# Optimization experiments

Measured on AMD Instinct MI355X. Metric: run time of the kernel, lower is better.

Reference implementation:

```python
import jax, jax.numpy as jnp
import numpy as np

B, C, H, W = 16, 512, 32, 32
GROUPS = 8
EPS = 1e-5


def setup_inputs() -> dict:
    key = jax.random.key(0)
    ks = jax.random.split(key, 7)
    s = 1.0 / np.sqrt(C)
    return {
        "x": jax.random.normal(ks[0], (B, C, H, W), dtype=jnp.float32),
        "gamma": jnp.ones((C,), dtype=jnp.float32),
        "beta": jnp.zeros((C,), dtype=jnp.float32),
        "w_qkv": jax.random.normal(ks[1], (3 * C, C), dtype=jnp.float32) * s,
        "b_qkv": jnp.zeros((3 * C,), dtype=jnp.float32),
        "w_proj": jax.random.normal(ks[2], (C, C), dtype=jnp.float32) * s,
        "b_proj": jnp.zeros((C,), dtype=jnp.float32),
    }


def group_norm(x, gamma, beta):
    b, c, h, w = x.shape
    xg = x.reshape(b, GROUPS, c // GROUPS, h, w)
    mean = xg.mean(axis=(2, 3, 4), keepdims=True)
    var = xg.var(axis=(2, 3, 4), keepdims=True)
    xn = ((xg - mean) * jax.lax.rsqrt(var + EPS)).reshape(b, c, h, w)
    return xn * gamma[None, :, None, None] + beta[None, :, None, None]


def reference(x, gamma, beta, w_qkv, b_qkv, w_proj, b_proj):
    b, c, h, w = x.shape
    n = h * w
    hn = group_norm(x, gamma, beta)
    # 1x1 conv == channel matmul: [3C, C] x [B, C, N] -> [B, 3C, N]
    qkv = jnp.einsum('oc,bcn->bon', w_qkv, hn.reshape(b, c, n)) + b_qkv[None, :, None]
    q, k, v = jnp.split(qkv, 3, axis=1)  # each [B, C, N]
    scale = c ** (-0.5)
    # scores [B, N, N]: q^T k
    attn = jax.nn.softmax(jnp.einsum('bcn,bcm->bnm', q, k) * scale, axis=-1)
    out = jnp.einsum('bnm,bcm->bcn', attn, v)  # [B, C, N]
    proj = jnp.einsum('oc,bcn->bon', w_proj, out) + b_proj[None, :, None]
    return x + proj.reshape(b, c, h, w)
```

## Files before the change

kernel.cpp:

```cpp
#include <hip/hip_runtime.h>


#define BATCH 16
#define CCH 512
#define NSP 1024
#define EPSV 1e-5f
#define BK 32
#define HT 4096

typedef short bf16x8 __attribute__((ext_vector_type(8)));
typedef float f32x4 __attribute__((ext_vector_type(4)));

__device__ __forceinline__ unsigned short f2bf(float f) {
    unsigned int u = __float_as_uint(f);
    u += 0x7FFF + ((u >> 16) & 1);
    return (unsigned short)(u >> 16);
}

__device__ __forceinline__ void glds16(const void* g, void* l) {
    __builtin_amdgcn_global_load_lds(
        (const __attribute__((address_space(1))) unsigned int*)g,
        (__attribute__((address_space(3))) unsigned int*)l, 16, 0, 0);
}

#define MEMF asm volatile("" ::: "memory")
#define VMW(n) asm volatile("s_waitcnt vmcnt(" #n ")" ::: "memory")

#define XCD_MAP(GX_LOG2, PER, xv, yv, bv)                 \
    const int lin_ = blockIdx.x;                          \
    const int xcd_ = lin_ & 7;                            \
    int slot_ = lin_ >> 3;                                \
    const int hi_ = (slot_ >= (PER)) ? 1 : 0;             \
    const int bv = xcd_ + 8 * hi_;                        \
    slot_ -= hi_ * (PER);                                 \
    const int xv = slot_ & ((1 << (GX_LOG2)) - 1);        \
    const int yv = slot_ >> (GX_LOG2);

__device__ __forceinline__ void gemm128_loop(
    const unsigned short* __restrict__ Ag, const unsigned short* __restrict__ Bg,
    int astr, int bstr, int ktot, short* Al, short* Bl, f32x4* acc) {
    const int t = threadIdx.x;
    const int w = t >> 6, lane = t & 63;
    const int wr = (w >> 1) * 64, wc = (w & 1) * 64;
    const int fr = lane & 15;
    const int fsw = (((lane >> 4) ^ (fr & 3)) * 8);
    const int r0 = t >> 2;
    const int kc = (((t & 3) ^ (r0 & 3)) * 8);
    const unsigned short* Ap0 = Ag + (size_t)r0 * astr + kc;
    const unsigned short* Ap1 = Ag + (size_t)(r0 + 64) * astr + kc;
    const unsigned short* Bp0 = Bg + (size_t)r0 * bstr + kc;
    const unsigned short* Bp1 = Bg + (size_t)(r0 + 64) * bstr + kc;
    short* Alw = Al + w * 512;
    short* Blw = Bl + w * 512;
    for (int k0 = 0; k0 < ktot; k0 += 64) {
        glds16(Ap0 + k0, Alw);
        glds16(Ap1 + k0, Alw + 2048);
        glds16(Ap0 + k0 + 32, Alw + HT);
        glds16(Ap1 + k0 + 32, Alw + HT + 2048);
        glds16(Bp0 + k0, Blw);
        glds16(Bp1 + k0, Blw + 2048);
        glds16(Bp0 + k0 + 32, Blw + HT);
        glds16(Bp1 + k0 + 32, Blw + HT + 2048);
        __syncthreads();
#pragma unroll
        for (int h = 0; h < 2; h++) {
            const short* Ab = Al + h * HT;
            const short* Bb = Bl + h * HT;
            bf16x8 af[4], bfr[4];
#pragma unroll
            for (int mi = 0; mi < 4; mi++)
                af[mi] = *(const bf16x8*)(Ab + (wr + mi * 16 + fr) * BK + fsw);
#pragma unroll
            for (int ni = 0; ni < 4; ni++)
                bfr[ni] = *(const bf16x8*)(Bb + (wc + ni * 16 + fr) * BK + fsw);
#pragma unroll
            for (int mi = 0; mi < 4; mi++)
#pragma unroll
                for (int ni = 0; ni < 4; ni++)
                    acc[mi * 4 + ni] = __builtin_amdgcn_mfma_f32_16x16x32_bf16(
                        af[mi], bfr[ni], acc[mi * 4 + ni], 0, 0, 0);
        }
        __syncthreads();
    }
}

__device__ __forceinline__ void gemm128_dbuf(
    const unsigned short* __restrict__ Ag, const unsigned short* __restrict__ Bg,
    int astr, int bstr, int ktot, short* L, f32x4* acc) {
    const int t = threadIdx.x;
    const int w = t >> 6, lane = t & 63;
    const int wr = (w >> 1) * 64, wc = (w & 1) * 64;
    const int fr = lane & 15;
    const int fsw = (((lane >> 4) ^ (fr & 3)) * 8);
    const int r0 = t >> 2;
    const int kc = (((t & 3) ^ (r0 & 3)) * 8);
    const unsigned short* Ap0 = Ag + (size_t)r0 * astr + kc;
    const unsigned short* Ap1 = Ag + (size_t)(r0 + 64) * astr + kc;
    const unsigned short* Bp0 = Bg + (size_t)r0 * bstr + kc;
    const unsigned short* Bp1 = Bg + (size_t)(r0 + 64) * bstr + kc;
    short* lw = L + w * 512;

#define STG(bf, kk) do {                                  \
    short* aw_ = lw + (bf) * (4 * HT);                    \
    short* bw_ = aw_ + 2 * HT;                            \
    glds16(Ap0 + (kk), aw_);                              \
    glds16(Ap1 + (kk), aw_ + 2048);                       \
    glds16(Ap0 + (kk) + 32, aw_ + HT);                    \
    glds16(Ap1 + (kk) + 32, aw_ + HT + 2048);             \
    glds16(Bp0 + (kk), bw_);                              \
    glds16(Bp1 + (kk), bw_ + 2048);                       \
    glds16(Bp0 + (kk) + 32, bw_ + HT);                    \
    glds16(Bp1 + (kk) + 32, bw_ + HT + 2048);             \
  } while (0)

#define CMP(bf) do {                                                        \
    _Pragma("unroll")                                                       \
    for (int h = 0; h < 2; h++) {                                           \
        const short* Ab_ = L + (bf) * (4 * HT) + h * HT;                    \
        const short* Bb_ = Ab_ + 2 * HT;                                    \
        bf16x8 af[4], bfr[4];                                               \
        _Pragma("unroll")                                                   \
        for (int mi = 0; mi < 4; mi++)                                      \
            af[mi] = *(const bf16x8*)(Ab_ + (wr + mi * 16 + fr) * BK + fsw);\
        _Pragma("unroll")                                                   \
        for (int ni = 0; ni < 4; ni++)                                      \
            bfr[ni] = *(const bf16x8*)(Bb_ + (wc + ni * 16 + fr) * BK + fsw);\
        _Pragma("unroll")                                                   \
        for (int mi = 0; mi < 4; mi++)                                      \
            _Pragma("unroll")                                               \
            for (int ni = 0; ni < 4; ni++)                                  \
                acc[mi * 4 + ni] = __builtin_amdgcn_mfma_f32_16x16x32_bf16( \
                    af[mi], bfr[ni], acc[mi * 4 + ni], 0, 0, 0);            \
    } } while (0)

    STG(0, 0);
    for (int k0 = 0; k0 < ktot; k0 += 128) {
        STG(1, k0 + 64);
        VMW(8);
        MEMF; __builtin_amdgcn_s_barrier();
        CMP(0);
        MEMF; __builtin_amdgcn_s_barrier();
        const int kb = (k0 + 128 < ktot) ? k0 + 128 : 0;
        STG(0, kb);
        VMW(8);
        MEMF; __builtin_amdgcn_s_barrier();
        CMP(1);
        MEMF; __builtin_amdgcn_s_barrier();
    }
    VMW(0);
#undef STG
#undef CMP
}

#define EPI_SETUP()                                          \
    const int t = threadIdx.x, lane = t & 63, w = t >> 6;    \
    const int wr = (w >> 1) * 64, wc = (w & 1) * 64;         \
    const int fr = lane & 15, rr0 = (lane >> 4) * 4;

#define ACC_INIT(acc)                                        \
    f32x4 acc[16];                                           \
    _Pragma("unroll") for (int i = 0; i < 16; i++)           \
        acc[i] = (f32x4){0.f, 0.f, 0.f, 0.f};

__global__ __launch_bounds__(256) void setup_k(
    const float* __restrict__ x, float* __restrict__ sp,
    const float* __restrict__ wa, unsigned short* __restrict__ oa, int na4,
    const float* __restrict__ wb, unsigned short* __restrict__ ob, int nb4,
    float* __restrict__ Lsum, const float* __restrict__ bqv,
    unsigned short* __restrict__ wv_t, float* __restrict__ puv) {
    const int t = threadIdx.x;
    const int bx = blockIdx.x;
    __shared__ float rs[4], rq[4];
    __shared__ __align__(16) unsigned short Tt[64 * 72];
    if (bx < 512) {
        const int bg = bx >> 2, q = bx & 3;
        const float4* xp = (const float4*)(x + (size_t)bg * 65536 + q * 16384);
        float s = 0.f, qq = 0.f;
#pragma unroll
        for (int i = 0; i < 16; i++) {
            float4 v = xp[t + i * 256];
            s += v.x + v.y + v.z + v.w;
            qq += v.x * v.x + v.y * v.y + v.z * v.z + v.w * v.w;
        }
#pragma unroll
        for (int off = 32; off; off >>= 1) {
            s += __shfl_down(s, off);
            qq += __shfl_down(qq, off);
        }
        const int wave = t >> 6, lane = t & 63;
        if (lane == 0) { rs[wave] = s; rq[wave] = qq; }
        __syncthreads();
        if (t == 0) {
            sp[bx * 2] = rs[0] + rs[1] + rs[2] + rs[3];
            sp[bx * 2 + 1] = rq[0] + rq[1] + rq[2] + rq[3];
        }
    } else if (bx < 1280) {
        int i = (bx - 512) * 256 + t;
        const float* src;
        unsigned short* dst;
        int j;
        if (i < na4) { src = wa; dst = oa; j = i; }
        else { j = i - na4; if (j >= nb4) return; src = wb; dst = ob; }
        float4 v = ((const float4*)src)[j];
        ushort4 o;
        o.x = f2bf(v.x); o.y = f2bf(v.y); o.z = f2bf(v.z); o.w = f2bf(v.w);
        ((ushort4*)dst)[j] = o;
    } else if (bx < 1296) {
        int i = (bx - 1280) * 256 + t;
        ((float4*)Lsum)[i] = (float4){0.f, 0.f, 0.f, 0.f};
    } else if (bx < 1360) {
        const int r = bx - 1296;
        const float* src = wa + (size_t)2 * 512 * 512;
        const int to = (r >> 3) * 64, tc = (r & 7) * 64;
        const int ol = t >> 2, cs = t & 3;
#pragma unroll
        for (int j = 0; j < 4; j++) {
            float4 v = *(const float4*)(src + (size_t)(to + ol) * 512 + tc + cs * 16 + j * 4);
            int c = cs * 16 + j * 4;
            Tt[(c + 0) * 72 + ol] = f2bf(v.x);
            Tt[(c + 1) * 72 + ol] = f2bf(v.y);
            Tt[(c + 2) * 72 + ol] = f2bf(v.z);
            Tt[(c + 3) * 72 + ol] = f2bf(v.w);
        }
        __syncthreads();
        const int cl = t >> 2, os = t & 3;
        unsigned short* d = wv_t + (size_t)(tc + cl) * 512 + to + os * 16;
        const unsigned short* s2 = Tt + cl * 72 + os * 16;
        *(uint4*)d = *(const uint4*)s2;
        *(uint4*)(d + 8) = *(const uint4*)(s2 + 8);
    } else {
        const int o = (bx - 1360) * 256 + t;
        const float* wr_ = wb + (size_t)o * 512;
        const float* bv = bqv + 1024;
        float s = 0.f;
        for (int vv = 0; vv < 512; vv += 4) {
            s += wr_[vv] * bv[vv] + wr_[vv + 1] * bv[vv + 1]
               + wr_[vv + 2] * bv[vv + 2] + wr_[vv + 3] * bv[vv + 3];
        }
        puv[o] = s;
    }
}

__global__ __launch_bounds__(256) void gn_tr_k(
    const float* __restrict__ x, const float* __restrict__ gamma,
    const float* __restrict__ beta, const float* __restrict__ sp,
    unsigned short* __restrict__ hn_t,
    const unsigned short* __restrict__ wp_bf, const unsigned short* __restrict__ wv_t,
    unsigned short* __restrict__ wpv_bf) {
    __shared__ __align__(16) short SM[4 * HT];
    const int lin = blockIdx.x;
    const int t = threadIdx.x;
    if (lin < 16) {
        const int ot = (lin >> 2) * 128, ct2 = (lin & 3) * 128;
        ACC_INIT(acc);
        gemm128_loop(wp_bf + (size_t)ot * 512, wv_t + (size_t)ct2 * 512,
                     512, 512, 512, SM, SM + 2 * HT, acc);
        EPI_SETUP();
#pragma unroll
        for (int ni = 0; ni < 4; ni++) {
            int col = ct2 + wc + ni * 16 + fr;
#pragma unroll
            for (int mi = 0; mi < 4; mi++) {
                int row = ot + wr + mi * 16 + rr0;
#pragma unroll
                for (int r = 0; r < 4; r++)
                    wpv_bf[(size_t)(row + r) * 512 + col] = f2bf(acc[mi * 4 + ni][r]);
            }
        }
        return;
    }
    const int l2 = lin - 16;
    const int nt = l2 & 15, ct = (l2 >> 4) & 7, b = l2 >> 7;
    unsigned short* T = (unsigned short*)SM;
    const int bg = b * 8 + ct;
    float S = 0.f, Q = 0.f;
#pragma unroll
    for (int qq = 0; qq < 4; qq++) {
        S += sp[(bg * 4 + qq) * 2];
        Q += sp[(bg * 4 + qq) * 2 + 1];
    }
    const float inv = 1.f / 65536.f;
    const float mean = S * inv;
    const float rstd = rsqrtf(Q * inv - mean * mean + EPSV);
    const int cl = t >> 2, nc = t & 3;
    const int c = ct * 64 + cl;
    const float ga = gamma[c] * rstd;
    const float be = beta[c] - mean * ga;
    const float4* xp = (const float4*)(x + ((size_t)b * CCH + c) * NSP + nt * 64);
#pragma unroll
    for (int j = 0; j < 4; j++) {
        float4 v = xp[nc * 4 + j];
        int n = nc * 16 + j * 4;
        T[(n + 0) * 72 + cl] = f2bf(v.x * ga + be);
        T[(n + 1) * 72 + cl] = f2bf(v.y * ga + be);
        T[(n + 2) * 72 + cl] = f2bf(v.z * ga + be);
        T[(n + 3) * 72 + cl] = f2bf(v.w * ga + be);
    }
    __syncthreads();
    const int nl = t >> 2, cc = t & 3;
    unsigned short* dst = hn_t + ((size_t)b * NSP + nt * 64 + nl) * CCH + ct * 64 + cc * 16;
    const unsigned short* src = T + nl * 72 + cc * 16;
    *(uint4*)dst = *(const uint4*)src;
    *(uint4*)(dst + 8) = *(const uint4*)(src + 8);
}

__global__ __launch_bounds__(256) void gemm_qku_k(
    const unsigned short* __restrict__ hn_t, const unsigned short* __restrict__ wq,
    const float* __restrict__ bq, const unsigned short* __restrict__ wpv_bf,
    const float* __restrict__ puv, unsigned short* __restrict__ QKt,
    unsigned short* __restrict__ Ub) {
    __shared__ __align__(16) short Al[2 * HT], Bl[2 * HT];
    XCD_MAP(3, 96, xb, y, b);
    const int ntc = xb * 128;
    ACC_INIT(acc);
    if (y < 8) {
        const int mt = y * 128;
        gemm128_loop(hn_t + ((size_t)b * NSP + mt) * CCH,
                     wq + (size_t)ntc * CCH, CCH, CCH, CCH, Al, Bl, acc);
        unsigned short* Ob = QKt + (size_t)b * NSP * 1024;
        EPI_SETUP();
#pragma unroll
        for (int ni = 0; ni < 4; ni++) {
            int col = ntc + wc + ni * 16 + fr;
            float bias = bq[col];
#pragma unroll
            for (int mi = 0; mi < 4; mi++) {
                int row = mt + wr + mi * 16 + rr0;
#pragma unroll
                for (int r = 0; r < 4; r++)
                    Ob[(size_t)(row + r) * 1024 + col] = f2bf(acc[mi * 4 + ni][r] + bias);
            }
        }
    } else {
        const int mt = (y - 8) * 128;
        gemm128_loop(wpv_bf + (size_t)mt * 512,
                     hn_t + ((size_t)b * NSP + ntc) * CCH, 512, CCH, 512, Al, Bl, acc);
        unsigned short* Ob = Ub + (size_t)b * CCH * NSP;
        EPI_SETUP();
#pragma unroll
        for (int mi = 0; mi < 4; mi++) {
            int row = mt + wr + mi * 16 + rr0;
#pragma unroll
            for (int r = 0; r < 4; r++) {
                float bias = puv[row + r];
#pragma unroll
                for (int ni = 0; ni < 4; ni++) {
                    int col = ntc + wc + ni * 16 + fr;
                    Ob[(size_t)(row + r) * NSP + col] = f2bf(acc[mi * 4 + ni][r] + bias);
                }
            }
        }
    }
}

__global__ __launch_bounds__(256) void gemm_scores_k(
    const unsigned short* __restrict__ QKt, unsigned short* __restrict__ expS,
    float* __restrict__ Lsum) {
    __shared__ __align__(16) short Al[2 * HT], Bl[2 * HT];
    XCD_MAP(3, 64, xb, yb, b);
    const int nt = xb * 128, mt = yb * 128;
    const unsigned short* base = QKt + (size_t)b * NSP * 1024;
    ACC_INIT(acc);
    gemm128_loop(base + (size_t)mt * 1024, base + (size_t)nt * 1024 + 512,
                 1024, 1024, 512, Al, Bl, acc);
    unsigned short* Ob = expS + (size_t)b * NSP * NSP;
    float* Ls = Lsum + (size_t)b * NSP;
    const float scale = 0.044194173824159216f;
    EPI_SETUP();
#pragma unroll
    for (int mi = 0; mi < 4; mi++) {
#pragma unroll
        for (int r = 0; r < 4; r++) {
            const int row = mt + wr + mi * 16 + rr0 + r;
            float rs = 0.f;
#pragma unroll
            for (int ni = 0; ni < 4; ni++) {
                int col = nt + wc + ni * 16 + fr;
                float e = __expf(acc[mi * 4 + ni][r] * scale);
                Ob[(size_t)row * NSP + col] = f2bf(e);
                rs += e;
            }
            rs += __shfl_xor(rs, 1);
            rs += __shfl_xor(rs, 2);
            rs += __shfl_xor(rs, 4);
            rs += __shfl_xor(rs, 8);
            if (fr == 0) atomicAdd(&Ls[row], rs);
        }
    }
}

__global__ __launch_bounds__(256) void gemm_pu_k(
    const unsigned short* __restrict__ Ub, const unsigned short* __restrict__ expS,
    const float* __restrict__ Lsum, const float* __restrict__ x,
    const float* __restrict__ bp, float* __restrict__ out) {
    __shared__ __align__(16) short L[8 * HT];
    XCD_MAP(3, 32, xb, yb, b);
    const int nt = xb * 128, ot = yb * 128;
    ACC_INIT(acc);
    gemm128_dbuf(Ub + ((size_t)b * CCH + ot) * NSP,
                 expS + ((size_t)b * NSP + nt) * NSP, NSP, NSP, NSP, L, acc);
    const float* Ls = Lsum + (size_t)b * NSP;
    const size_t bbase = (size_t)b * CCH * NSP;
    EPI_SETUP();
#pragma unroll
    for (int ni = 0; ni < 4; ni++) {
        int col = nt + wc + ni * 16 + fr;
        float invl = __builtin_amdgcn_rcpf(Ls[col]);
#pragma unroll
        for (int mi = 0; mi < 4; mi++) {
            int row = ot + wr + mi * 16 + rr0;
#pragma unroll
            for (int r = 0; r < 4; r++) {
                size_t idx = bbase + (size_t)(row + r) * NSP + col;
                out[idx] = x[idx] + bp[row + r] + acc[mi * 4 + ni][r] * invl;
            }
        }
    }
}

extern "C" void kernel_launch(void* const* d_in, const int* in_sizes, int n_in,
                              void* d_out, int out_size, void* d_ws, size_t ws_size,
                              hipStream_t stream) {
    const float* x = (const float*)d_in[0];
    const float* gamma = (const float*)d_in[1];
    const float* beta = (const float*)d_in[2];
    const float* w_qkv = (const float*)d_in[3];
    const float* b_qkv = (const float*)d_in[4];
    const float* w_proj = (const float*)d_in[5];
    const float* b_proj = (const float*)d_in[6];
    float* out = (float*)d_out;

    char* ws = (char*)d_ws;
    const size_t MB = 1048576;
    const size_t KB = 1024;
    unsigned short* wqkv_bf = (unsigned short*)ws;
    unsigned short* wproj_bf = (unsigned short*)(ws + 1572864);
    float* sp = (float*)(ws + 2 * MB);
    float* Lsum = (float*)(ws + 2 * MB + 64 * KB);
    float* puv = (float*)(ws + 2 * MB + 128 * KB);
    unsigned short* wv_t = (unsigned short*)(ws + 2 * MB + 256 * KB);
    unsigned short* wpv_bf = (unsigned short*)(ws + 3 * MB);
    unsigned short* hn_t = (unsigned short*)(ws + 4 * MB);
    unsigned short* QKt = (unsigned short*)(ws + 24 * MB);
    unsigned short* Ub = (unsigned short*)(ws + 60 * MB);
    unsigned short* expS = (unsigned short*)(ws + 80 * MB);

    setup_k<<<1362, 256, 0, stream>>>(x, sp, w_qkv, wqkv_bf, 131072,
                                      w_proj, wproj_bf, 65536, Lsum, b_qkv,
                                      wv_t, puv);
    gn_tr_k<<<2064, 256, 0, stream>>>(x, gamma, beta, sp, hn_t,
                                      wproj_bf, wv_t, wpv_bf);
    gemm_qku_k<<<1536, 256, 0, stream>>>(hn_t, wqkv_bf, b_qkv, wpv_bf, puv,
                                         QKt, Ub);
    gemm_scores_k<<<1024, 256, 0, stream>>>(QKt, expS, Lsum);
    gemm_pu_k<<<512, 256, 0, stream>>>(Ub, expS, Lsum, x, b_proj, out);
}
```

Measured before the change: 212.1 us.

## Switch scores and PU GEMMs to 128x64 single-buffered tiles with more blocks

Replaces the 128x128 double-buffered GEMM mainloop in the scores and output-projection kernels with a 128x64 tile and a simple single-buffered loop, cutting LDS use and accumulator registers. Grid sizes double and the XCD mapping is adjusted. The intent is higher occupancy and better load balance across CUs. The cost is more global traffic per FLOP and no overlap between loads and compute in the PU GEMM.

```diff
diff --git a/kernel.cpp b/kernel.cpp
--- a/kernel.cpp
+++ b/kernel.cpp
@@ -22,9 +22,6 @@
         (const __attribute__((address_space(1))) unsigned int*)g,
         (__attribute__((address_space(3))) unsigned int*)l, 16, 0, 0);
 }
-
-#define MEMF asm volatile("" ::: "memory")
-#define VMW(n) asm volatile("s_waitcnt vmcnt(" #n ")" ::: "memory")
 
 #define XCD_MAP(GX_LOG2, PER, xv, yv, bv)                 \
     const int lin_ = blockIdx.x;                          \
@@ -84,12 +81,12 @@
     }
 }
 
-__device__ __forceinline__ void gemm128_dbuf(
+__device__ __forceinline__ void gemm12864_sb(
     const unsigned short* __restrict__ Ag, const unsigned short* __restrict__ Bg,
     int astr, int bstr, int ktot, short* L, f32x4* acc) {
     const int t = threadIdx.x;
     const int w = t >> 6, lane = t & 63;
-    const int wr = (w >> 1) * 64, wc = (w & 1) * 64;
+    const int wr = (w >> 1) * 64, wc = (w & 1) * 32;
     const int fr = lane & 15;
     const int fsw = (((lane >> 4) ^ (fr & 3)) * 8);
     const int r0 = t >> 2;
@@ -97,59 +94,36 @@
     const unsigned short* Ap0 = Ag + (size_t)r0 * astr + kc;
     const unsigned short* Ap1 = Ag + (size_t)(r0 + 64) * astr + kc;
     const unsigned short* Bp0 = Bg + (size_t)r0 * bstr + kc;
-    const unsigned short* Bp1 = Bg + (size_t)(r0 + 64) * bstr + kc;
-    short* lw = L + w * 512;
-
-#define STG(bf, kk) do {                                  \
-    short* aw_ = lw + (bf) * (4 * HT);                    \
-    short* bw_ = aw_ + 2 * HT;                            \
-    glds16(Ap0 + (kk), aw_);                              \
-    glds16(Ap1 + (kk), aw_ + 2048);                       \
-    glds16(Ap0 + (kk) + 32, aw_ + HT);                    \
-    glds16(Ap1 + (kk) + 32, aw_ + HT + 2048);             \
-    glds16(Bp0 + (kk), bw_);                              \
-    glds16(Bp1 + (kk), bw_ + 2048);                       \
-    glds16(Bp0 + (kk) + 32, bw_ + HT);                    \
-    glds16(Bp1 + (kk) + 32, bw_ + HT + 2048);             \
-  } while (0)
-
-#define CMP(bf) do {                                                        \
-    _Pragma("unroll")                                                       \
-    for (int h = 0; h < 2; h++) {                                           \
-        const short* Ab_ = L + (bf) * (4 * HT) + h * HT;                    \
-        const short* Bb_ = Ab_ + 2 * HT;                                    \
-        bf16x8 af[4], bfr[4];                                               \
-        _Pragma("unroll")                                                   \
-        for (int mi = 0; mi < 4; mi++)                                      \
-            af[mi] = *(const bf16x8*)(Ab_ + (wr + mi * 16 + fr) * BK + fsw);\
-        _Pragma("unroll")                                                   \
-        for (int ni = 0; ni < 4; ni++)                                      \
-            bfr[ni] = *(const bf16x8*)(Bb_ + (wc + ni * 16 + fr) * BK + fsw);\
-        _Pragma("unroll")                                                   \
-        for (int mi = 0; mi < 4; mi++)                                      \
-            _Pragma("unroll")                                               \
-            for (int ni = 0; ni < 4; ni++)                                  \
-                acc[mi * 4 + ni] = __builtin_amdgcn_mfma_f32_16x16x32_bf16( \
-                    af[mi], bfr[ni], acc[mi * 4 + ni], 0, 0, 0);            \
-    } } while (0)
-
-    STG(0, 0);
-    for (int k0 = 0; k0 < ktot; k0 += 128) {
-        STG(1, k0 + 64);
-        VMW(8);
-        MEMF; __builtin_amdgcn_s_barrier();
-        CMP(0);
-        MEMF; __builtin_amdgcn_s_barrier();
-        const int kb = (k0 + 128 < ktot) ? k0 + 128 : 0;
-        STG(0, kb);
-        VMW(8);
-        MEMF; __builtin_amdgcn_s_barrier();
-        CMP(1);
-        MEMF; __builtin_amdgcn_s_barrier();
-    }
-    VMW(0);
-#undef STG
-#undef CMP
+    short* Alw = L + w * 512;
+    short* Blw = L + 8192 + w * 512;
+    for (int k0 = 0; k0 < ktot; k0 += 64) {
+        glds16(Ap0 + k0, Alw);
+        glds16(Ap1 + k0, Alw + 2048);
+        glds16(Ap0 + k0 + 32, Alw + 4096);
+        glds16(Ap1 + k0 + 32, Alw + 4096 + 2048);
+        glds16(Bp0 + k0, Blw);
+        glds16(Bp0 + k0 + 32, Blw + 2048);
+        __syncthreads();
+#pragma unroll
+        for (int h = 0; h < 2; h++) {
+            const short* Ab = L + h * 4096;
+            const short* Bb = L + 8192 + h * 2048;
+            bf16x8 af[4], bfr[2];
+#pragma unroll
+            for (int mi = 0; mi < 4; mi++)
+                af[mi] = *(const bf16x8*)(Ab + (wr + mi * 16 + fr) * 32 + fsw);
+#pragma unroll
+            for (int ni = 0; ni < 2; ni++)
+                bfr[ni] = *(const bf16x8*)(Bb + (wc + ni * 16 + fr) * 32 + fsw);
+#pragma unroll
+            for (int mi = 0; mi < 4; mi++)
+#pragma unroll
+                for (int ni = 0; ni < 2; ni++)
+                    acc[mi * 2 + ni] = __builtin_amdgcn_mfma_f32_16x16x32_bf16(
+                        af[mi], bfr[ni], acc[mi * 2 + ni], 0, 0, 0);
+        }
+        __syncthreads();
+    }
 }
 
 #define EPI_SETUP()                                          \
@@ -157,9 +131,19 @@
     const int wr = (w >> 1) * 64, wc = (w & 1) * 64;         \
     const int fr = lane & 15, rr0 = (lane >> 4) * 4;
 
+#define EPI_SETUP64()                                        \
+    const int t = threadIdx.x, lane = t & 63, w = t >> 6;    \
+    const int wr = (w >> 1) * 64, wc = (w & 1) * 32;         \
+    const int fr = lane & 15, rr0 = (lane >> 4) * 4;
+
 #define ACC_INIT(acc)                                        \
     f32x4 acc[16];                                           \
     _Pragma("unroll") for (int i = 0; i < 16; i++)           \
+        acc[i] = (f32x4){0.f, 0.f, 0.f, 0.f};
+
+#define ACC_INIT8(acc)                                       \
+    f32x4 acc[8];                                            \
+    _Pragma("unroll") for (int i = 0; i < 8; i++)            \
         acc[i] = (f32x4){0.f, 0.f, 0.f, 0.f};
 
 __global__ __launch_bounds__(256) void setup_k(
@@ -356,17 +340,17 @@
 __global__ __launch_bounds__(256) void gemm_scores_k(
     const unsigned short* __restrict__ QKt, unsigned short* __restrict__ expS,
     float* __restrict__ Lsum) {
-    __shared__ __align__(16) short Al[2 * HT], Bl[2 * HT];
-    XCD_MAP(3, 64, xb, yb, b);
-    const int nt = xb * 128, mt = yb * 128;
+    __shared__ __align__(16) short L[12288];
+    XCD_MAP(4, 128, xb, yb, b);
+    const int nt = xb * 64, mt = yb * 128;
     const unsigned short* base = QKt + (size_t)b * NSP * 1024;
-    ACC_INIT(acc);
-    gemm128_loop(base + (size_t)mt * 1024, base + (size_t)nt * 1024 + 512,
-                 1024, 1024, 512, Al, Bl, acc);
+    ACC_INIT8(acc);
+    gemm12864_sb(base + (size_t)mt * 1024, base + (size_t)nt * 1024 + 512,
+                 1024, 1024, 512, L, acc);
     unsigned short* Ob = expS + (size_t)b * NSP * NSP;
     float* Ls = Lsum + (size_t)b * NSP;
     const float scale = 0.044194173824159216f;
-    EPI_SETUP();
+    EPI_SETUP64();
 #pragma unroll
     for (int mi = 0; mi < 4; mi++) {
 #pragma unroll
@@ -374,9 +358,9 @@
             const int row = mt + wr + mi * 16 + rr0 + r;
             float rs = 0.f;
 #pragma unroll
-            for (int ni = 0; ni < 4; ni++) {
+            for (int ni = 0; ni < 2; ni++) {
                 int col = nt + wc + ni * 16 + fr;
-                float e = __expf(acc[mi * 4 + ni][r] * scale);
+                float e = __expf(acc[mi * 2 + ni][r] * scale);
                 Ob[(size_t)row * NSP + col] = f2bf(e);
                 rs += e;
             }
@@ -393,17 +377,17 @@
     const unsigned short* __restrict__ Ub, const unsigned short* __restrict__ expS,
     const float* __restrict__ Lsum, const float* __restrict__ x,
     const float* __restrict__ bp, float* __restrict__ out) {
-    __shared__ __align__(16) short L[8 * HT];
-    XCD_MAP(3, 32, xb, yb, b);
-    const int nt = xb * 128, ot = yb * 128;
-    ACC_INIT(acc);
-    gemm128_dbuf(Ub + ((size_t)b * CCH + ot) * NSP,
+    __shared__ __align__(16) short L[12288];
+    XCD_MAP(4, 64, xb, yb, b);
+    const int nt = xb * 64, ot = yb * 128;
+    ACC_INIT8(acc);
+    gemm12864_sb(Ub + ((size_t)b * CCH + ot) * NSP,
                  expS + ((size_t)b * NSP + nt) * NSP, NSP, NSP, NSP, L, acc);
     const float* Ls = Lsum + (size_t)b * NSP;
     const size_t bbase = (size_t)b * CCH * NSP;
-    EPI_SETUP();
-#pragma unroll
-    for (int ni = 0; ni < 4; ni++) {
+    EPI_SETUP64();
+#pragma unroll
+    for (int ni = 0; ni < 2; ni++) {
         int col = nt + wc + ni * 16 + fr;
         float invl = __builtin_amdgcn_rcpf(Ls[col]);
 #pragma unroll
@@ -412,7 +396,7 @@
 #pragma unroll
             for (int r = 0; r < 4; r++) {
                 size_t idx = bbase + (size_t)(row + r) * NSP + col;
-                out[idx] = x[idx] + bp[row + r] + acc[mi * 4 + ni][r] * invl;
+                out[idx] = x[idx] + bp[row + r] + acc[mi * 2 + ni][r] * invl;
             }
         }
     }
@@ -452,6 +436,6 @@
                                       wproj_bf, wv_t, wpv_bf);
     gemm_qku_k<<<1536, 256, 0, stream>>>(hn_t, wqkv_bf, b_qkv, wpv_bf, puv,
                                          QKt, Ub);
-    gemm_scores_k<<<1024, 256, 0, stream>>>(QKt, expS, Lsum);
-    gemm_pu_k<<<512, 256, 0, stream>>>(Ub, expS, Lsum, x, b_proj, out);
-}
+    gemm_scores_k<<<2048, 256, 0, stream>>>(QKt, expS, Lsum);
+    gemm_pu_k<<<1024, 256, 0, stream>>>(Ub, expS, Lsum, x, b_proj, out);
+}
```

Result: slower. 226.0 us (+6.6%).
